# Kernel tuning notes

Measured on AMD Instinct MI355X. Metric: run time of the kernel, lower is better.

Reference implementation:

```python
import jax, jax.numpy as jnp
import numpy as np

D_MODEL, D_K, D_V = 1024, 128, 128
B, S = 4, 2048

def setup_inputs() -> dict:
    key = jax.random.key(0)
    k1, k2, k3, k4 = jax.random.split(key, 4)
    return {
        "x_q": jax.random.normal(k1, (B, S, D_MODEL), dtype=jnp.float32),
        "w_q": jax.random.normal(k2, (D_MODEL, D_K), dtype=jnp.float32),
        "w_k": jax.random.normal(k3, (D_MODEL, D_K), dtype=jnp.float32),
        "w_v": jax.random.normal(k4, (D_MODEL, D_V), dtype=jnp.float32),
    }

def reference(x_q, w_q, w_k, w_v):
    # Self-attention: x_k = x_v = x_q (module defaults)
    Q = x_q @ w_q            # [B,S,d_k]
    K = x_q @ w_k            # [B,S,d_k]
    V = x_q @ w_v            # [B,S,d_v]
    scores = jnp.einsum('bqd,bkd->bqk', Q, K) / jnp.sqrt(jnp.float32(D_K))
    # causal mask: tril (row i attends to cols j <= i)
    causal = jnp.tril(jnp.ones((S, S), dtype=bool))
    scores = jnp.where(causal, scores, -jnp.inf)
    # NOTE: softmax over dim=-2 (query axis), per original module
    attention = jax.nn.softmax(scores, axis=-2)
    out = jnp.einsum('bqk,bkv->bqv', attention, V)
    return out, attention
```

## Files before the change

kernel.cpp:

```cpp
#include <hip/hip_runtime.h>
#include <math.h>
#include <stdint.h>

#define B_ 4
#define S_ 2048
#define DM_ 1024
#define DK_ 128

static constexpr float SCALE = 0.08838834764831845f;

typedef __attribute__((ext_vector_type(8))) short short8;
typedef __attribute__((ext_vector_type(4))) float f32x4;
typedef __attribute__((ext_vector_type(4))) unsigned short us4;

__device__ __forceinline__ unsigned enc_f32(float f){
  unsigned u = __float_as_uint(f);
  return (u & 0x80000000u) ? ~u : (u | 0x80000000u);
}
__device__ __forceinline__ float dec_f32(unsigned u){
  unsigned v = (u & 0x80000000u) ? (u & 0x7FFFFFFFu) : ~u;
  return __uint_as_float(v);
}
__device__ __forceinline__ unsigned short bf16rne(float f){
  unsigned u = __float_as_uint(f);
  unsigned r = (u + 0x7FFFu + ((u>>16)&1u)) >> 16;
  return (unsigned short)r;
}
__device__ __forceinline__ float bf16tof(unsigned short h){
  return __uint_as_float((unsigned)h << 16);
}
__device__ __forceinline__ void gload16(const void* g, void* l){
  __builtin_amdgcn_global_load_lds(
      (const __attribute__((address_space(1))) void*)g,
      (__attribute__((address_space(3))) void*)l, 16, 0, 0);
}

__global__ __launch_bounds__(256) void init_kernel(unsigned* __restrict__ cmax){
  int i = blockIdx.x*256 + threadIdx.x;
  if(i < B_*S_) cmax[i] = 0x007FFFFFu;
}

__global__ __launch_bounds__(256) void xconv_kernel(
    const float* __restrict__ X,
    unsigned short* __restrict__ Xth, unsigned short* __restrict__ Xtl)
{
  const int kt = blockIdx.x & 31, mb = blockIdx.x >> 5;
  const int tid = threadIdx.x;
  const int unit = tid & 127, half = tid >> 7;
  const int g = unit >> 5, row = unit & 31;
  const float* src = X + (size_t)(mb*32 + row)*DM_ + kt*32 + g*8;
  float4 a = *reinterpret_cast<const float4*>(src);
  float4 b = *reinterpret_cast<const float4*>(src + 4);
  unsigned short* dst = (half ? Xtl : Xth) + ((size_t)(mb*32 + kt)*128 + unit)*8;
  if(half == 0){
    us4 h0 = {bf16rne(a.x),bf16rne(a.y),bf16rne(a.z),bf16rne(a.w)};
    us4 h1 = {bf16rne(b.x),bf16rne(b.y),bf16rne(b.z),bf16rne(b.w)};
    *(us4*)dst = h0; *(us4*)(dst+4) = h1;
  } else {
    us4 l0 = {bf16rne(a.x - bf16tof(bf16rne(a.x))), bf16rne(a.y - bf16tof(bf16rne(a.y))),
              bf16rne(a.z - bf16tof(bf16rne(a.z))), bf16rne(a.w - bf16tof(bf16rne(a.w)))};
    us4 l1 = {bf16rne(b.x - bf16tof(bf16rne(b.x))), bf16rne(b.y - bf16tof(bf16rne(b.y))),
              bf16rne(b.z - bf16tof(bf16rne(b.z))), bf16rne(b.w - bf16tof(bf16rne(b.w)))};
    *(us4*)dst = l0; *(us4*)(dst+4) = l1;
  }
}

__global__ __launch_bounds__(256) void wconv_kernel(
    const float* __restrict__ Wq, const float* __restrict__ Wk, const float* __restrict__ Wv,
    unsigned short* __restrict__ Wth, unsigned short* __restrict__ Wtl)
{
  const int t = blockIdx.x;
  const int which = blockIdx.y;
  const float* W = (which==0) ? Wq : ((which==1) ? Wk : Wv);
  const int tid = threadIdx.x;
  const size_t obase = ((size_t)which*32 + t)*5120;
  #pragma unroll
  for(int it=0; it<2; ++it){
    int idx = tid + 256*it;
    int col = idx & 127, g = idx >> 7;
    unsigned short hs[8], ls[8];
    #pragma unroll
    for(int j=0;j<8;j++){
      float f = W[(size_t)(t*32 + g*8 + j)*DK_ + col];
      unsigned short h = bf16rne(f);
      hs[j] = h;
      ls[j] = bf16rne(f - bf16tof(h));
    }
    size_t o = obase + (size_t)col*40 + g*8;
    *(us4*)&Wth[o]   = us4{hs[0],hs[1],hs[2],hs[3]};
    *(us4*)&Wth[o+4] = us4{hs[4],hs[5],hs[6],hs[7]};
    *(us4*)&Wtl[o]   = us4{ls[0],ls[1],ls[2],ls[3]};
    *(us4*)&Wtl[o+4] = us4{ls[4],ls[5],ls[6],ls[7]};
  }
}

__global__ __launch_bounds__(256) void qkv_mfma_kernel(
    const unsigned short* __restrict__ Xth, const unsigned short* __restrict__ Xtl,
    const unsigned short* __restrict__ Wth, const unsigned short* __restrict__ Wtl,
    unsigned short* __restrict__ Qh, unsigned short* __restrict__ Ql,
    unsigned short* __restrict__ Kh, unsigned short* __restrict__ Kl,
    unsigned short* __restrict__ Vth, unsigned short* __restrict__ Vtl)
{
  __shared__ __align__(16) unsigned char smem[49152];
  const int tid = threadIdx.x;
  const int w = tid >> 6, lane = tid & 63;
  const int l15 = lane & 15, g = lane >> 4;
  const int which = blockIdx.y;
  const int m0 = blockIdx.x * 32;
  const int mb = blockIdx.x;
  const unsigned char* Wh8 = (const unsigned char*)(Wth + (size_t)which*32*5120);
  const unsigned char* Wl8 = (const unsigned char*)(Wtl + (size_t)which*32*5120);
  const unsigned short* Asrc = ((w < 2) ? Xth : Xtl) + (size_t)(mb*32)*1024 + (w & 1)*512 + lane*8;
  const unsigned Adst = (unsigned)((w & 1)*1024) + ((w < 2) ? 0u : 2048u);

  gload16(Asrc, smem + Adst + lane*0  );
  #pragma unroll
  for(int ii=0; ii<5; ++ii){
    int i = w + 4*ii;
    const unsigned char* src = (i<10) ? (Wh8 + i*1024) : (Wl8 + (i-10)*1024);
    unsigned dst = 8192u + ((i<10) ? (unsigned)i*1024u : 10240u + (unsigned)(i-10)*1024u);
    gload16(src + lane*16, smem + dst);
  }

  f32x4 acc[4] = {f32x4{0,0,0,0},f32x4{0,0,0,0},f32x4{0,0,0,0},f32x4{0,0,0,0}};
  const int r = w >> 1, c0 = (w & 1)*4;
  const int aoff = (g*32 + r*16 + l15)*8;
  int buf = 0;
  for(int t=0; t<32; ++t){
    __syncthreads();
    if(t+1 < 32){
      gload16(Asrc + (size_t)(t+1)*1024, smem + (buf^1)*4096 + Adst);
      const unsigned char* WhT = Wh8 + (size_t)(t+1)*10240;
      const unsigned char* WlT = Wl8 + (size_t)(t+1)*10240;
      unsigned bbase = 8192u + (unsigned)(buf^1)*20480u;
      #pragma unroll
      for(int ii=0; ii<5; ++ii){
        int i = w + 4*ii;
        const unsigned char* src = (i<10) ? (WhT + i*1024) : (WlT + (i-10)*1024);
        unsigned dst = bbase + ((i<10) ? (unsigned)i*1024u : 10240u + (unsigned)(i-10)*1024u);
        gload16(src + lane*16, smem + dst);
      }
    }
    const unsigned short* Ab = (const unsigned short*)(smem + buf*4096);
    const unsigned short* Bhc = (const unsigned short*)(smem + 8192 + buf*20480);
    const unsigned short* Blc = Bhc + 5120;
    short8 ah = *(const short8*)&Ab[aoff];
    short8 al = *(const short8*)&Ab[1024 + aoff];
    #pragma unroll
    for(int c=0;c<4;c++){
      int boff = ((c0+c)*16 + l15)*40 + g*8;
      short8 bh = *(const short8*)&Bhc[boff];
      short8 bl = *(const short8*)&Blc[boff];
      acc[c] = __builtin_amdgcn_mfma_f32_16x16x32_bf16(ah, bh, acc[c], 0, 0, 0);
      acc[c] = __builtin_amdgcn_mfma_f32_16x16x32_bf16(ah, bl, acc[c], 0, 0, 0);
      acc[c] = __builtin_amdgcn_mfma_f32_16x16x32_bf16(al, bh, acc[c], 0, 0, 0);
    }
    buf ^= 1;
  }
  const int b = m0 >> 11;
  const int orow0 = g*4;
  if(which != 2){
    unsigned short* Oh = (which==0) ? Qh : Kh;
    unsigned short* Ol = (which==0) ? Ql : Kl;
    #pragma unroll
    for(int c=0;c<4;c++){
      int col = (c0+c)*16 + l15;
      #pragma unroll
      for(int j=0;j<4;j++){
        float f = acc[c][j];
        unsigned short h = bf16rne(f);
        unsigned short lo = bf16rne(f - bf16tof(h));
        size_t o = (size_t)(m0 + r*16 + orow0 + j)*DK_ + col;
        Oh[o] = h; Ol[o] = lo;
      }
    }
  } else {
    __syncthreads();
    float* Tmp = (float*)smem;
    #pragma unroll
    for(int c=0;c<4;c++){
      int col = (c0+c)*16 + l15;
      #pragma unroll
      for(int j=0;j<4;j++)
        Tmp[(r*16 + orow0 + j)*133 + col] = acc[c][j];
    }
    __syncthreads();
    const int s0 = m0 & (S_-1);
    #pragma unroll
    for(int l2=0;l2<16;l2++){
      int p = tid + 256*l2;
      int d = p >> 5, rr = p & 31;
      float f = Tmp[rr*133 + d];
      unsigned short h = bf16rne(f);
      Vth[(size_t)(b*DK_ + d)*S_ + s0 + rr] = h;
      Vtl[(size_t)(b*DK_ + d)*S_ + s0 + rr] = bf16rne(f - bf16tof(h));
    }
  }
}

__global__ __launch_bounds__(256) void scores_kernel(
    const unsigned short* __restrict__ Qh, const unsigned short* __restrict__ Ql,
    const unsigned short* __restrict__ Kh, const unsigned short* __restrict__ Kl,
    float* __restrict__ attn, unsigned* __restrict__ cmax)
{
  const int tj = blockIdx.x, ti = blockIdx.y, b = blockIdx.z;
  const int tid = threadIdx.x;
  const int q0 = ti*64, k0 = tj*64;
  if(tj > ti){
    float4 z = {0.f,0.f,0.f,0.f};
    #pragma unroll
    for(int l=0;l<4;l++){
      int p = tid + 256*l;
      int r = p >> 4, c = (p & 15) << 2;
      *reinterpret_cast<float4*>(&attn[((size_t)(b*S_) + q0 + r)*S_ + k0 + c]) = z;
    }
    return;
  }
  __shared__ __align__(16) unsigned short sm[18432];
  __shared__ float cred[16][64];
  unsigned short* Qhs = sm;
  unsigned short* Qls = sm + 4608;
  unsigned short* Khs = sm + 9216;
  unsigned short* Kls = sm + 13824;
  const int w = tid >> 6, lane = tid & 63, l15 = lane & 15, g = lane >> 4;
  f32x4 acc[4] = {f32x4{0,0,0,0},f32x4{0,0,0,0},f32x4{0,0,0,0},f32x4{0,0,0,0}};
  for(int kh=0; kh<2; ++kh){
    __syncthreads();
    #pragma unroll
    for(int l=0;l<2;l++){
      int p = tid + 256*l;
      int row = p >> 3, cc = p & 7;
      size_t gq = (size_t)(b*S_ + q0 + row)*DK_ + kh*64 + cc*8;
      size_t gk = (size_t)(b*S_ + k0 + row)*DK_ + kh*64 + cc*8;
      int lo_ = row*72 + cc*8;
      *(short8*)&Qhs[lo_] = *(const short8*)&Qh[gq];
      *(short8*)&Qls[lo_] = *(const short8*)&Ql[gq];
      *(short8*)&Khs[lo_] = *(const short8*)&Kh[gk];
      *(short8*)&Kls[lo_] = *(const short8*)&Kl[gk];
    }
    __syncthreads();
    #pragma unroll
    for(int ks=0; ks<2; ++ks){
      int ao = (w*16 + l15)*72 + ks*32 + g*8;
      short8 ah = *(const short8*)&Qhs[ao];
      short8 al = *(const short8*)&Qls[ao];
      #pragma unroll
      for(int c=0;c<4;c++){
        int bo = (c*16 + l15)*72 + ks*32 + g*8;
        short8 bh = *(const short8*)&Khs[bo];
        short8 bl = *(const short8*)&Kls[bo];
        acc[c] = __builtin_amdgcn_mfma_f32_16x16x32_bf16(ah, bh, acc[c], 0, 0, 0);
        acc[c] = __builtin_amdgcn_mfma_f32_16x16x32_bf16(ah, bl, acc[c], 0, 0, 0);
        acc[c] = __builtin_amdgcn_mfma_f32_16x16x32_bf16(al, bh, acc[c], 0, 0, 0);
      }
    }
  }
  const bool full = (ti > tj);
  const int qbase = q0 + w*16 + g*4;
  #pragma unroll
  for(int c=0;c<4;c++){
    int kcol = k0 + c*16 + l15;
    float cm = -INFINITY;
    #pragma unroll
    for(int j=0;j<4;j++){
      int q = qbase + j;
      float s = acc[c][j]*SCALE;
      bool valid = full || (q >= kcol);
      attn[((size_t)(b*S_) + q)*S_ + kcol] = valid ? s : 0.f;
      if(valid) cm = fmaxf(cm, s);
    }
    cred[w*4 + g][c*16 + l15] = cm;
  }
  __syncthreads();
  if(tid < 64){
    float m = cred[0][tid];
    #pragma unroll
    for(int gg=1;gg<16;gg++) m = fmaxf(m, cred[gg][tid]);
    atomicMax(&cmax[b*S_ + k0 + tid], enc_f32(m));
  }
}

__global__ __launch_bounds__(256) void expsum_kernel(
    const float* __restrict__ attn, const unsigned* __restrict__ cmax,
    float* __restrict__ colpart)
{
  const int cj = blockIdx.x, ti = blockIdx.y, b = blockIdx.z;
  if(ti < 4*cj) return;
  __shared__ float part[4][256];
  const int tid = threadIdx.x;
  const int c4 = tid & 63, g = tid >> 6;
  const int q0 = ti*64, k0 = cj*256;
  const int kbase = k0 + c4*4;
  float mc[4];
  #pragma unroll
  for(int j=0;j<4;j++) mc[j] = dec_f32(cmax[b*S_ + kbase + j]);
  float sum[4] = {0.f,0.f,0.f,0.f};
  #pragma unroll 4
  for(int rr=0;rr<16;rr++){
    int q = q0 + g*16 + rr;
    size_t idx = ((size_t)(b*S_) + q)*S_ + kbase;
    float4 sv = *reinterpret_cast<const float4*>(&attn[idx]);
    sum[0] += (q >= kbase+0) ? __expf(sv.x - mc[0]) : 0.f;
    sum[1] += (q >= kbase+1) ? __expf(sv.y - mc[1]) : 0.f;
    sum[2] += (q >= kbase+2) ? __expf(sv.z - mc[2]) : 0.f;
    sum[3] += (q >= kbase+3) ? __expf(sv.w - mc[3]) : 0.f;
  }
  #pragma unroll
  for(int j=0;j<4;j++) part[g][c4*4+j] = sum[j];
  __syncthreads();
  {
    int k = k0 + tid;
    float tot = ((part[0][tid] + part[1][tid]) + part[2][tid]) + part[3][tid];
    colpart[((size_t)(b*S_) + k)*32 + ti] = tot;
  }
}

__global__ __launch_bounds__(256) void colreduce_kernel(
    const float* __restrict__ colpart, float* __restrict__ rcol)
{
  int i = blockIdx.x*256 + threadIdx.x;
  if(i >= B_*S_) return;
  int k = i & (S_-1);
  int t0 = k >> 6;
  float s = 0.f;
  for(int t=t0; t<32; t++) s += colpart[(size_t)i*32 + t];
  rcol[i] = 1.0f / s;
}

__global__ __launch_bounds__(256) void pv_kernel(
    float* __restrict__ attn, const unsigned* __restrict__ cmax,
    const float* __restrict__ rcol,
    const unsigned short* __restrict__ Vth, const unsigned short* __restrict__ Vtl,
    float* __restrict__ part, int ns)
{
  __shared__ __align__(16) unsigned short sm[27648];
  unsigned short* Ahs = sm;
  unsigned short* Als = sm + 4608;
  unsigned short* Vhs = sm + 9216;
  unsigned short* Vls = sm + 18432;
  const int b = blockIdx.z, tid = threadIdx.x;
  const int sp = blockIdx.y;
  const int w = tid >> 6, lane = tid & 63, l15 = lane & 15, g = lane >> 4;
  const int t = 31 - (int)blockIdx.x;
  const int q0 = t*64;
  const int nch = t + 1;
  const int lo = (sp*nch)/ns, hi = ((sp+1)*nch)/ns;
  f32x4 acc[8] = {f32x4{0,0,0,0},f32x4{0,0,0,0},f32x4{0,0,0,0},f32x4{0,0,0,0},
                  f32x4{0,0,0,0},f32x4{0,0,0,0},f32x4{0,0,0,0},f32x4{0,0,0,0}};
  const int er = tid >> 4, ekq = (tid & 15) << 2;
  for(int ch=lo; ch<hi; ++ch){
    const int k0c = ch*64;
    uint4 mu = *reinterpret_cast<const uint4*>(&cmax[b*S_ + k0c + ekq]);
    float4 r4 = *reinterpret_cast<const float4*>(&rcol[b*S_ + k0c + ekq]);
    float mc0 = dec_f32(mu.x), mc1 = dec_f32(mu.y), mc2 = dec_f32(mu.z), mc3 = dec_f32(mu.w);
    const bool diag = (ch == t);
    __syncthreads();
    #pragma unroll
    for(int rr=0; rr<4; ++rr){
      int row = rr*16 + er;
      size_t ea = ((size_t)(b*S_) + q0 + row)*S_ + k0c + ekq;
      float4 sv = *reinterpret_cast<const float4*>(&attn[ea]);
      float p0 = __expf(sv.x - mc0)*r4.x;
      float p1 = __expf(sv.y - mc1)*r4.y;
      float p2 = __expf(sv.z - mc2)*r4.z;
      float p3 = __expf(sv.w - mc3)*r4.w;
      if(diag){
        p0 = (row >= ekq+0) ? p0 : 0.f;
        p1 = (row >= ekq+1) ? p1 : 0.f;
        p2 = (row >= ekq+2) ? p2 : 0.f;
        p3 = (row >= ekq+3) ? p3 : 0.f;
      }
      float4 pv4 = {p0,p1,p2,p3};
      *reinterpret_cast<float4*>(&attn[ea]) = pv4;
      unsigned short h0=bf16rne(p0), h1=bf16rne(p1), h2=bf16rne(p2), h3=bf16rne(p3);
      *(us4*)&Ahs[row*72 + ekq] = us4{h0,h1,h2,h3};
      *(us4*)&Als[row*72 + ekq] = us4{ bf16rne(p0-bf16tof(h0)), bf16rne(p1-bf16tof(h1)),
                                       bf16rne(p2-bf16tof(h2)), bf16rne(p3-bf16tof(h3)) };
    }
    #pragma unroll
    for(int v=0; v<4; ++v){
      int idx = v*256 + tid;
      int d = idx >> 3, c8 = (idx & 7) << 3;
      size_t ga = (size_t)(b*DK_ + d)*S_ + k0c + c8;
      *(short8*)&Vhs[d*72 + c8] = *(const short8*)&Vth[ga];
      *(short8*)&Vls[d*72 + c8] = *(const short8*)&Vtl[ga];
    }
    __syncthreads();
    #pragma unroll
    for(int ks=0; ks<2; ++ks){
      int ao = (w*16 + l15)*72 + ks*32 + g*8;
      short8 ah = *(const short8*)&Ahs[ao];
      short8 al = *(const short8*)&Als[ao];
      #pragma unroll
      for(int c=0;c<8;c++){
        int bo = (c*16 + l15)*72 + ks*32 + g*8;
        short8 bh = *(const short8*)&Vhs[bo];
        short8 bl = *(const short8*)&Vls[bo];
        acc[c] = __builtin_amdgcn_mfma_f32_16x16x32_bf16(ah, bh, acc[c], 0, 0, 0);
        acc[c] = __builtin_amdgcn_mfma_f32_16x16x32_bf16(ah, bl, acc[c], 0, 0, 0);
        acc[c] = __builtin_amdgcn_mfma_f32_16x16x32_bf16(al, bh, acc[c], 0, 0, 0);
      }
    }
  }
  float* pout = part + (((size_t)(sp*B_ + b))*S_ + q0)*DK_;
  #pragma unroll
  for(int c=0;c<8;c++){
    #pragma unroll
    for(int j=0;j<4;j++){
      int qrow = w*16 + g*4 + j;
      pout[(size_t)qrow*DK_ + c*16 + l15] = acc[c][j];
    }
  }
}

__global__ __launch_bounds__(256) void pvreduce_kernel(
    const float* __restrict__ part, float* __restrict__ out, int ns)
{
  const int N4 = (B_*S_*DK_)/4;
  int i = blockIdx.x*256 + threadIdx.x;
  if(i >= N4) return;
  const float4* p = reinterpret_cast<const float4*>(part);
  float4 a = p[i];
  for(int s=1; s<ns; ++s){
    float4 q = p[(size_t)s*N4 + i];
    a.x += q.x; a.y += q.y; a.z += q.z; a.w += q.w;
  }
  reinterpret_cast<float4*>(out)[i] = a;
}

extern "C" void kernel_launch(void* const* d_in, const int* in_sizes, int n_in,
                              void* d_out, int out_size, void* d_ws, size_t ws_size,
                              hipStream_t stream)
{
  (void)in_sizes; (void)n_in; (void)out_size;
  const float* X  = (const float*)d_in[0];
  const float* Wq = (const float*)d_in[1];
  const float* Wk = (const float*)d_in[2];
  const float* Wv = (const float*)d_in[3];
  float* out  = (float*)d_out;
  float* attn = out + (size_t)B_*S_*DK_;

  unsigned short* Xth = (unsigned short*)attn;
  unsigned short* Xtl = Xth + (size_t)8388608;

  float* ws = (float*)d_ws;
  unsigned* cmax = (unsigned*)ws;
  float* rcol    = ws + 8192;
  float* colpart = ws + 16384;
  unsigned short* Wth = (unsigned short*)(ws + 278528);
  unsigned short* Wtl = (unsigned short*)(ws + 524288);
  unsigned short* Qh  = (unsigned short*)(ws + 770048);
  unsigned short* Ql  = (unsigned short*)(ws + 1294336);
  unsigned short* Kh  = (unsigned short*)(ws + 1818624);
  unsigned short* Kl  = (unsigned short*)(ws + 2342912);
  unsigned short* Vth = (unsigned short*)(ws + 2867200);
  unsigned short* Vtl = (unsigned short*)(ws + 3391488);
  const size_t base = 3915776;
  float* part    = ws + base;

  int ns = 4;
  if(ws_size < (base + (size_t)4*1048576)*sizeof(float)) ns = 2;
  if(ws_size < (base + (size_t)2*1048576)*sizeof(float)) ns = 1;

  init_kernel<<<dim3(32), dim3(256), 0, stream>>>(cmax);
  xconv_kernel<<<dim3(8192), dim3(256), 0, stream>>>(X, Xth, Xtl);
  wconv_kernel<<<dim3(32,3), dim3(256), 0, stream>>>(Wq, Wk, Wv, Wth, Wtl);
  qkv_mfma_kernel<<<dim3(256,3), dim3(256), 0, stream>>>(Xth, Xtl, Wth, Wtl, Qh, Ql, Kh, Kl, Vth, Vtl);
  scores_kernel<<<dim3(32,32,4), dim3(256), 0, stream>>>(Qh, Ql, Kh, Kl, attn, cmax);
  expsum_kernel<<<dim3(8,32,4), dim3(256), 0, stream>>>(attn, cmax, colpart);
  colreduce_kernel<<<dim3(32), dim3(256), 0, stream>>>(colpart, rcol);
  pv_kernel<<<dim3(32,ns,4), dim3(256), 0, stream>>>(attn, cmax, rcol, Vth, Vtl, part, ns);
  pvreduce_kernel<<<dim3(1024), dim3(256), 0, stream>>>(part, out, ns);
}
```

Baseline: 124.7 us.

## Fuse column exp-sum into scores kernel using online per-tile max rescaling

Measured after the change: 121.3 us. 2.7% less time.

```diff
diff --git a/kernel.cpp b/kernel.cpp
--- a/kernel.cpp
+++ b/kernel.cpp
@@ -13,14 +13,6 @@
 typedef __attribute__((ext_vector_type(4))) float f32x4;
 typedef __attribute__((ext_vector_type(4))) unsigned short us4;
 
-__device__ __forceinline__ unsigned enc_f32(float f){
-  unsigned u = __float_as_uint(f);
-  return (u & 0x80000000u) ? ~u : (u | 0x80000000u);
-}
-__device__ __forceinline__ float dec_f32(unsigned u){
-  unsigned v = (u & 0x80000000u) ? (u & 0x7FFFFFFFu) : ~u;
-  return __uint_as_float(v);
-}
 __device__ __forceinline__ unsigned short bf16rne(float f){
   unsigned u = __float_as_uint(f);
   unsigned r = (u + 0x7FFFu + ((u>>16)&1u)) >> 16;
@@ -33,11 +25,6 @@
   __builtin_amdgcn_global_load_lds(
       (const __attribute__((address_space(1))) void*)g,
       (__attribute__((address_space(3))) void*)l, 16, 0, 0);
-}
-
-__global__ __launch_bounds__(256) void init_kernel(unsigned* __restrict__ cmax){
-  int i = blockIdx.x*256 + threadIdx.x;
-  if(i < B_*S_) cmax[i] = 0x007FFFFFu;
 }
 
 __global__ __launch_bounds__(256) void xconv_kernel(
@@ -113,7 +100,7 @@
   const unsigned short* Asrc = ((w < 2) ? Xth : Xtl) + (size_t)(mb*32)*1024 + (w & 1)*512 + lane*8;
   const unsigned Adst = (unsigned)((w & 1)*1024) + ((w < 2) ? 0u : 2048u);
 
-  gload16(Asrc, smem + Adst + lane*0  );
+  gload16(Asrc, smem + Adst);
   #pragma unroll
   for(int ii=0; ii<5; ++ii){
     int i = w + 4*ii;
@@ -201,7 +188,7 @@
 __global__ __launch_bounds__(256) void scores_kernel(
     const unsigned short* __restrict__ Qh, const unsigned short* __restrict__ Ql,
     const unsigned short* __restrict__ Kh, const unsigned short* __restrict__ Kl,
-    float* __restrict__ attn, unsigned* __restrict__ cmax)
+    float* __restrict__ attn, float* __restrict__ cmaxpart, float* __restrict__ csumpart)
 {
   const int tj = blockIdx.x, ti = blockIdx.y, b = blockIdx.z;
   const int tid = threadIdx.x;
@@ -218,6 +205,8 @@
   }
   __shared__ __align__(16) unsigned short sm[18432];
   __shared__ float cred[16][64];
+  __shared__ float csum[16][64];
+  __shared__ float maxsh[64];
   unsigned short* Qhs = sm;
   unsigned short* Qls = sm + 4608;
   unsigned short* Khs = sm + 9216;
@@ -276,59 +265,51 @@
     float m = cred[0][tid];
     #pragma unroll
     for(int gg=1;gg<16;gg++) m = fmaxf(m, cred[gg][tid]);
-    atomicMax(&cmax[b*S_ + k0 + tid], enc_f32(m));
-  }
-}
-
-__global__ __launch_bounds__(256) void expsum_kernel(
-    const float* __restrict__ attn, const unsigned* __restrict__ cmax,
-    float* __restrict__ colpart)
-{
-  const int cj = blockIdx.x, ti = blockIdx.y, b = blockIdx.z;
-  if(ti < 4*cj) return;
-  __shared__ float part[4][256];
-  const int tid = threadIdx.x;
-  const int c4 = tid & 63, g = tid >> 6;
-  const int q0 = ti*64, k0 = cj*256;
-  const int kbase = k0 + c4*4;
-  float mc[4];
+    maxsh[tid] = m;
+    cmaxpart[((size_t)(b*S_) + k0 + tid)*32 + ti] = m;
+  }
+  __syncthreads();
   #pragma unroll
-  for(int j=0;j<4;j++) mc[j] = dec_f32(cmax[b*S_ + kbase + j]);
-  float sum[4] = {0.f,0.f,0.f,0.f};
-  #pragma unroll 4
-  for(int rr=0;rr<16;rr++){
-    int q = q0 + g*16 + rr;
-    size_t idx = ((size_t)(b*S_) + q)*S_ + kbase;
-    float4 sv = *reinterpret_cast<const float4*>(&attn[idx]);
-    sum[0] += (q >= kbase+0) ? __expf(sv.x - mc[0]) : 0.f;
-    sum[1] += (q >= kbase+1) ? __expf(sv.y - mc[1]) : 0.f;
-    sum[2] += (q >= kbase+2) ? __expf(sv.z - mc[2]) : 0.f;
-    sum[3] += (q >= kbase+3) ? __expf(sv.w - mc[3]) : 0.f;
-  }
-  #pragma unroll
-  for(int j=0;j<4;j++) part[g][c4*4+j] = sum[j];
+  for(int c=0;c<4;c++){
+    int col = c*16 + l15;
+    int kcol = k0 + col;
+    float mcol = maxsh[col];
+    float ps = 0.f;
+    #pragma unroll
+    for(int j=0;j<4;j++){
+      int q = qbase + j;
+      bool valid = full || (q >= kcol);
+      if(valid) ps += __expf(acc[c][j]*SCALE - mcol);
+    }
+    csum[w*4 + g][col] = ps;
+  }
   __syncthreads();
-  {
-    int k = k0 + tid;
-    float tot = ((part[0][tid] + part[1][tid]) + part[2][tid]) + part[3][tid];
-    colpart[((size_t)(b*S_) + k)*32 + ti] = tot;
+  if(tid < 64){
+    float s = 0.f;
+    #pragma unroll
+    for(int gg=0;gg<16;gg++) s += csum[gg][tid];
+    csumpart[((size_t)(b*S_) + k0 + tid)*32 + ti] = s;
   }
 }
 
 __global__ __launch_bounds__(256) void colreduce_kernel(
-    const float* __restrict__ colpart, float* __restrict__ rcol)
+    const float* __restrict__ cmaxpart, const float* __restrict__ csumpart,
+    float* __restrict__ cmaxf, float* __restrict__ rcol)
 {
   int i = blockIdx.x*256 + threadIdx.x;
   if(i >= B_*S_) return;
   int k = i & (S_-1);
   int t0 = k >> 6;
+  float M = -INFINITY;
+  for(int t=t0; t<32; t++) M = fmaxf(M, cmaxpart[(size_t)i*32 + t]);
   float s = 0.f;
-  for(int t=t0; t<32; t++) s += colpart[(size_t)i*32 + t];
+  for(int t=t0; t<32; t++) s += csumpart[(size_t)i*32 + t] * __expf(cmaxpart[(size_t)i*32 + t] - M);
+  cmaxf[i] = M;
   rcol[i] = 1.0f / s;
 }
 
 __global__ __launch_bounds__(256) void pv_kernel(
-    float* __restrict__ attn, const unsigned* __restrict__ cmax,
+    float* __restrict__ attn, const float* __restrict__ cmaxf,
     const float* __restrict__ rcol,
     const unsigned short* __restrict__ Vth, const unsigned short* __restrict__ Vtl,
     float* __restrict__ part, int ns)
@@ -350,9 +331,8 @@
   const int er = tid >> 4, ekq = (tid & 15) << 2;
   for(int ch=lo; ch<hi; ++ch){
     const int k0c = ch*64;
-    uint4 mu = *reinterpret_cast<const uint4*>(&cmax[b*S_ + k0c + ekq]);
+    float4 m4 = *reinterpret_cast<const float4*>(&cmaxf[b*S_ + k0c + ekq]);
     float4 r4 = *reinterpret_cast<const float4*>(&rcol[b*S_ + k0c + ekq]);
-    float mc0 = dec_f32(mu.x), mc1 = dec_f32(mu.y), mc2 = dec_f32(mu.z), mc3 = dec_f32(mu.w);
     const bool diag = (ch == t);
     __syncthreads();
     #pragma unroll
@@ -360,10 +340,10 @@
       int row = rr*16 + er;
       size_t ea = ((size_t)(b*S_) + q0 + row)*S_ + k0c + ekq;
       float4 sv = *reinterpret_cast<const float4*>(&attn[ea]);
-      float p0 = __expf(sv.x - mc0)*r4.x;
-      float p1 = __expf(sv.y - mc1)*r4.y;
-      float p2 = __expf(sv.z - mc2)*r4.z;
-      float p3 = __expf(sv.w - mc3)*r4.w;
+      float p0 = __expf(sv.x - m4.x)*r4.x;
+      float p1 = __expf(sv.y - m4.y)*r4.y;
+      float p2 = __expf(sv.z - m4.z)*r4.z;
+      float p3 = __expf(sv.w - m4.w)*r4.w;
       if(diag){
         p0 = (row >= ekq+0) ? p0 : 0.f;
         p1 = (row >= ekq+1) ? p1 : 0.f;
@@ -444,31 +424,30 @@
   unsigned short* Xtl = Xth + (size_t)8388608;
 
   float* ws = (float*)d_ws;
-  unsigned* cmax = (unsigned*)ws;
-  float* rcol    = ws + 8192;
-  float* colpart = ws + 16384;
-  unsigned short* Wth = (unsigned short*)(ws + 278528);
-  unsigned short* Wtl = (unsigned short*)(ws + 524288);
-  unsigned short* Qh  = (unsigned short*)(ws + 770048);
-  unsigned short* Ql  = (unsigned short*)(ws + 1294336);
-  unsigned short* Kh  = (unsigned short*)(ws + 1818624);
-  unsigned short* Kl  = (unsigned short*)(ws + 2342912);
-  unsigned short* Vth = (unsigned short*)(ws + 2867200);
-  unsigned short* Vtl = (unsigned short*)(ws + 3391488);
-  const size_t base = 3915776;
+  float* cmaxf    = ws;
+  float* rcol     = ws + 8192;
+  float* csumpart = ws + 16384;
+  float* cmaxpart = ws + 278528;
+  unsigned short* Wth = (unsigned short*)(ws + 540672);
+  unsigned short* Wtl = (unsigned short*)(ws + 786432);
+  unsigned short* Qh  = (unsigned short*)(ws + 1032192);
+  unsigned short* Ql  = (unsigned short*)(ws + 1556480);
+  unsigned short* Kh  = (unsigned short*)(ws + 2080768);
+  unsigned short* Kl  = (unsigned short*)(ws + 2605056);
+  unsigned short* Vth = (unsigned short*)(ws + 3129344);
+  unsigned short* Vtl = (unsigned short*)(ws + 3653632);
+  const size_t base = 4177920;
   float* part    = ws + base;
 
   int ns = 4;
   if(ws_size < (base + (size_t)4*1048576)*sizeof(float)) ns = 2;
   if(ws_size < (base + (size_t)2*1048576)*sizeof(float)) ns = 1;
 
-  init_kernel<<<dim3(32), dim3(256), 0, stream>>>(cmax);
   xconv_kernel<<<dim3(8192), dim3(256), 0, stream>>>(X, Xth, Xtl);
   wconv_kernel<<<dim3(32,3), dim3(256), 0, stream>>>(Wq, Wk, Wv, Wth, Wtl);
   qkv_mfma_kernel<<<dim3(256,3), dim3(256), 0, stream>>>(Xth, Xtl, Wth, Wtl, Qh, Ql, Kh, Kl, Vth, Vtl);
-  scores_kernel<<<dim3(32,32,4), dim3(256), 0, stream>>>(Qh, Ql, Kh, Kl, attn, cmax);
-  expsum_kernel<<<dim3(8,32,4), dim3(256), 0, stream>>>(attn, cmax, colpart);
-  colreduce_kernel<<<dim3(32), dim3(256), 0, stream>>>(colpart, rcol);
-  pv_kernel<<<dim3(32,ns,4), dim3(256), 0, stream>>>(attn, cmax, rcol, Vth, Vtl, part, ns);
+  scores_kernel<<<dim3(32,32,4), dim3(256), 0, stream>>>(Qh, Ql, Kh, Kl, attn, cmaxpart, csumpart);
+  colreduce_kernel<<<dim3(32), dim3(256), 0, stream>>>(cmaxpart, csumpart, cmaxf, rcol);
+  pv_kernel<<<dim3(32,ns,4), dim3(256), 0, stream>>>(attn, cmaxf, rcol, Vth, Vtl, part, ns);
   pvreduce_kernel<<<dim3(1024), dim3(256), 0, stream>>>(part, out, ns);
 }
```
